# Kernel tuning notes

Measured on AMD Instinct MI355X. Metric: run time of the kernel, lower is better.

Reference implementation:

```python
import jax, jax.numpy as jnp
import numpy as np

N = 50000      # nodes
E = 1600000    # edges (avg degree 32)
C = 48         # num_classes
S = 10         # num_steps


def setup_inputs() -> dict:
    key = jax.random.key(0)
    k1, k2, k3, k4 = jax.random.split(key, 4)
    edge_index = jax.random.randint(k1, (2, E), 0, N)
    edge_attr = jax.random.uniform(k2, (E,), dtype=jnp.float32)  # positive edge weights
    target = jax.random.randint(k3, (N,), 0, C)
    bound = 1.0 / np.sqrt(S)  # uniform(size, weight) init from PyG
    weight = jax.random.uniform(k4, (C, S), minval=-bound, maxval=bound, dtype=jnp.float32)
    return {"edge_index": edge_index, "edge_attr": edge_attr, "target": target, "weight": weight}


def reference(edge_index, edge_attr, target, weight):
    """Adaptive-diffusion random walk: propagate one-hot class indicators
    through a row-normalized weighted transition matrix for S steps and
    combine step-wise landing distributions with learned weight[c, s]."""
    row, col = edge_index[0], edge_index[1]
    # Row-normalize edge weights -> random-walk transition probabilities
    deg = jax.ops.segment_sum(edge_attr, row, num_segments=N)          # [N]
    norm = edge_attr / jnp.clip(deg, 1e-12)[row]                        # [E]
    h0 = jax.nn.one_hot(target, C, dtype=weight.dtype)                  # [N, C]

    def step(h, w_s):
        # message = P^T-style aggregation: scatter src features to dst
        h_new = jax.ops.segment_sum(norm[:, None] * h[row], col, num_segments=N)  # [N, C]
        return h_new, h_new * w_s  # w_s: [C], per-class step coefficient

    _, contribs = jax.lax.scan(step, h0, weight.T)  # contribs: [S, N, C]
    return contribs.sum(0)                          # [N, C]
```

## Files before the change

kernel.cpp:

```cpp
#include <hip/hip_runtime.h>
#include <hip/hip_fp16.h>

#define NN 50000
#define NE 1600000
#define NC 48
#define NS 10
#define PAD 88
#define PADN 50176

#define NBUCK 392
#define NB2   784
#define CAP   4608
#define EPB   2048
#define EPT   2

typedef __attribute__((ext_vector_type(8))) _Float16 half8;

__global__ __launch_bounds__(1024) void bin_kernel(const int* __restrict__ row,
        const int* __restrict__ col, const float* __restrict__ attr,
        int* __restrict__ bcur, uint2* __restrict__ bin, unsigned int* __restrict__ rbin) {
    __shared__ int hcnt[NB2];
    __shared__ int hbase[NB2];
    __shared__ int lofs[NB2];
    __shared__ int sc[1024];
    __shared__ uint2 stageC[EPB];
    __shared__ unsigned int stageR[EPB];
    int tid = threadIdx.x;
    if (tid < NB2) hcnt[tid] = 0;
    __syncthreads();
    int base = blockIdx.x * EPB;
    int ntot = min(EPB, NE - base);
    unsigned int rec[EPT];
    int cv[EPT];
    #pragma unroll
    for (int k = 0; k < EPT; ++k) {
        int e = base + k * 1024 + tid;
        if (e < NE) {
            int r = row[e], c = col[e];
            unsigned int iq = (unsigned int)rintf(attr[e] * 65535.0f);
            rec[k] = (iq << 16) | (unsigned int)r;
            cv[k] = c;
            atomicAdd(&hcnt[c >> 7], 1);
            atomicAdd(&hcnt[NBUCK + (r >> 7)], 1);
        } else {
            cv[k] = -1;
        }
    }
    __syncthreads();
    if (tid < NB2) hbase[tid] = atomicAdd(&bcur[tid], hcnt[tid]);
    sc[tid] = (tid < NB2) ? hcnt[tid] : 0;
    __syncthreads();
    for (int off = 1; off < 1024; off <<= 1) {
        int t = (tid >= off) ? sc[tid - off] : 0;
        __syncthreads();
        sc[tid] += t;
        __syncthreads();
    }
    if (tid < NB2) {
        lofs[tid] = sc[tid] - hcnt[tid];
        hcnt[tid] = 0;
    }
    __syncthreads();
    #pragma unroll
    for (int k = 0; k < EPT; ++k) {
        if (cv[k] >= 0) {
            int b = cv[k] >> 7;
            int rk = atomicAdd(&hcnt[b], 1);
            stageC[lofs[b] + rk] = make_uint2(rec[k], (unsigned int)cv[k]);
            int b2 = NBUCK + ((rec[k] & 0xffffu) >> 7);
            int rk2 = atomicAdd(&hcnt[b2], 1);
            stageR[lofs[b2] + rk2 - ntot] = rec[k];
        }
    }
    __syncthreads();
    for (int i = tid; i < ntot; i += 1024) {
        uint2 rc = stageC[i];
        int b = (int)(rc.y >> 7);
        bin[(size_t)b * CAP + hbase[b] + (i - lofs[b])] = rc;
    }
    for (int i = tid; i < ntot; i += 1024) {
        unsigned int rr = stageR[i];
        int b2 = NBUCK + ((rr & 0xffffu) >> 7);
        rbin[(size_t)(b2 - NBUCK) * CAP + hbase[b2] + (i + ntot - lofs[b2])] = rr;
    }
}

__global__ __launch_bounds__(1024) void degrdeg_kernel(const int* __restrict__ bcur,
        const unsigned int* __restrict__ rbin, const int* __restrict__ target,
        float* __restrict__ rdeg, int2* __restrict__ tq) {
    __shared__ unsigned int acc[128];
    int rb = blockIdx.x;
    if (threadIdx.x < 128) acc[threadIdx.x] = 0;
    __syncthreads();
    int n = bcur[NBUCK + rb];
    const unsigned int* rp = rbin + (size_t)rb * CAP;
    for (int i = threadIdx.x; i < n; i += 1024) {
        unsigned int rr = rp[i];
        atomicAdd(&acc[rr & 127], rr >> 16);
    }
    __syncthreads();
    if (threadIdx.x < 128) {
        int v = (rb << 7) + threadIdx.x;
        if (v < NN) {
            float rd = 65535.0f / fmaxf((float)acc[threadIdx.x], 1.0f);
            rdeg[v] = rd;
            tq[v] = make_int2(target[v], __float_as_int(rd));
        }
    }
}

__global__ __launch_bounds__(1024) void place_kernel(const int* __restrict__ bcur,
        const uint2* __restrict__ bin, unsigned int* __restrict__ edges,
        int* __restrict__ cnt) {
    __shared__ int ccnt[128];
    int b = blockIdx.x;
    if (threadIdx.x < 128) ccnt[threadIdx.x] = 0;
    __syncthreads();
    int n = bcur[b];
    const uint2* rp = bin + (size_t)b * CAP;
    for (int i = threadIdx.x; i < n; i += 1024) {
        uint2 r = rp[i];
        int c = (int)r.y;
        int pos = atomicAdd(&ccnt[c & 127], 1);
        edges[(size_t)c * PAD + pos] = r.x;
    }
    __syncthreads();
    if (threadIdx.x < 128) {
        int c = (b << 7) + threadIdx.x;
        if (c < NN) cnt[c] = ccnt[threadIdx.x];
    }
}

__global__ __launch_bounds__(256) void step1_kernel(const int* __restrict__ cnt,
        const unsigned int* __restrict__ edges, const int2* __restrict__ tq,
        const float* __restrict__ rdeg, const float* __restrict__ weight,
        _Float16* __restrict__ p_new, float* __restrict__ out) {
    int idx = blockIdx.x * blockDim.x + threadIdx.x;
    if (idx >= NN * 6) return;
    int v = idx / 6;
    int q = idx - v * 6;
    int n = cnt[v];
    const unsigned int* ep = edges + (size_t)v * PAD;
    int c0 = 8 * q;
    float a[8] = {0.f, 0.f, 0.f, 0.f, 0.f, 0.f, 0.f, 0.f};
    int i = 0;
    for (; i + 4 <= n; i += 4) {
        uint4 pa = *reinterpret_cast<const uint4*>(ep + i);
        int2 t0 = tq[pa.x & 0xffffu];
        int2 t1 = tq[pa.y & 0xffffu];
        int2 t2 = tq[pa.z & 0xffffu];
        int2 t3 = tq[pa.w & 0xffffu];
        float w0 = (float)(pa.x >> 16) * __int_as_float(t0.y);
        float w1 = (float)(pa.y >> 16) * __int_as_float(t1.y);
        float w2 = (float)(pa.z >> 16) * __int_as_float(t2.y);
        float w3 = (float)(pa.w >> 16) * __int_as_float(t3.y);
        int b0 = t0.x - c0, b1 = t1.x - c0, b2 = t2.x - c0, b3 = t3.x - c0;
        #pragma unroll
        for (int j = 0; j < 8; ++j) {
            a[j] += (b0 == j) ? w0 : 0.f;
            a[j] += (b1 == j) ? w1 : 0.f;
            a[j] += (b2 == j) ? w2 : 0.f;
            a[j] += (b3 == j) ? w3 : 0.f;
        }
    }
    for (; i < n; ++i) {
        unsigned int w_ = ep[i];
        int2 t0 = tq[w_ & 0xffffu];
        float w0 = (float)(w_ >> 16) * __int_as_float(t0.y);
        int b0 = t0.x - c0;
        #pragma unroll
        for (int j = 0; j < 8; ++j) a[j] += (b0 == j) ? w0 : 0.f;
    }
    #pragma unroll
    for (int j = 0; j < 8; ++j) a[j] *= (1.0f / 65535.0f);

    size_t off = (size_t)v * NC + c0;
    float w[8];
    #pragma unroll
    for (int j = 0; j < 8; ++j) w[j] = weight[(c0 + j) * NS + 0];
    *reinterpret_cast<float4*>(out + off) =
        make_float4(a[0] * w[0], a[1] * w[1], a[2] * w[2], a[3] * w[3]);
    *reinterpret_cast<float4*>(out + off + 4) =
        make_float4(a[4] * w[4], a[5] * w[5], a[6] * w[6], a[7] * w[7]);
    float rd = rdeg[v];
    half8 ph;
    #pragma unroll
    for (int j = 0; j < 8; ++j) ph[j] = (_Float16)(a[j] * rd);
    *reinterpret_cast<half8*>(p_new + off) = ph;
}

__device__ __forceinline__ void acc_edge(unsigned int w_, const char* pb, float* a) {
    const half8 g = *reinterpret_cast<const half8*>(pb + (w_ & 0xffffu) * (NC * 2));
    float wv = (float)(w_ >> 16) * (1.0f / 65535.0f);
    #pragma unroll
    for (int j = 0; j < 8; ++j) a[j] += wv * (float)g[j];
}

template <bool LAST>
__global__ __launch_bounds__(256) void gather_kernel(const int* __restrict__ cnt,
        const unsigned int* __restrict__ edges, const float* __restrict__ rdeg,
        const _Float16* __restrict__ p, _Float16* __restrict__ p_new,
        const float* __restrict__ weight, int t, float* __restrict__ out) {
    int idx = blockIdx.x * blockDim.x + threadIdx.x;
    if (idx >= NN * 6) return;
    int v = idx / 6;
    int q = idx - v * 6;
    int n = cnt[v];
    const unsigned int* ep = edges + (size_t)v * PAD;
    const char* pb = (const char*)p + q * 16;
    float a[8] = {0.f, 0.f, 0.f, 0.f, 0.f, 0.f, 0.f, 0.f};
    int i = 0;
    for (; i + 8 <= n; i += 8) {
        uint4 pa = *reinterpret_cast<const uint4*>(ep + i);
        uint4 pc = *reinterpret_cast<const uint4*>(ep + i + 4);
        acc_edge(pa.x, pb, a); acc_edge(pa.y, pb, a);
        acc_edge(pa.z, pb, a); acc_edge(pa.w, pb, a);
        acc_edge(pc.x, pb, a); acc_edge(pc.y, pb, a);
        acc_edge(pc.z, pb, a); acc_edge(pc.w, pb, a);
    }
    for (; i < n; ++i) acc_edge(ep[i], pb, a);

    size_t off = (size_t)v * NC + q * 8;
    int c0 = 8 * q;
    float w[8];
    #pragma unroll
    for (int j = 0; j < 8; ++j) w[j] = weight[(c0 + j) * NS + (t - 1)];
    float* op = out + off;
    float4 o0 = *reinterpret_cast<float4*>(op);
    float4 o1 = *reinterpret_cast<float4*>(op + 4);
    o0.x += a[0] * w[0]; o0.y += a[1] * w[1]; o0.z += a[2] * w[2]; o0.w += a[3] * w[3];
    o1.x += a[4] * w[4]; o1.y += a[5] * w[5]; o1.z += a[6] * w[6]; o1.w += a[7] * w[7];
    *reinterpret_cast<float4*>(op) = o0;
    *reinterpret_cast<float4*>(op + 4) = o1;
    if (!LAST) {
        float rd = rdeg[v];
        half8 ph;
        #pragma unroll
        for (int j = 0; j < 8; ++j) ph[j] = (_Float16)(a[j] * rd);
        *reinterpret_cast<half8*>(p_new + off) = ph;
    }
}

extern "C" void kernel_launch(void* const* d_in, const int* in_sizes, int n_in,
                              void* d_out, int out_size, void* d_ws, size_t ws_size,
                              hipStream_t stream) {
    const int*   edge_index = (const int*)d_in[0];
    const float* edge_attr  = (const float*)d_in[1];
    const int*   target     = (const int*)d_in[2];
    const float* weight     = (const float*)d_in[3];
    float* out = (float*)d_out;

    const int* row = edge_index;
    const int* col = edge_index + NE;

    float*        rdeg  = (float*)d_ws;
    int*          bcur  = (int*)(rdeg + PADN);
    int*          cnt   = bcur + 1024;
    int2*         tq    = (int2*)(cnt + PADN);
    unsigned int* edges = (unsigned int*)(tq + NN);
    unsigned int* rbin  = edges;
    uint2*        bin   = (uint2*)(edges + (size_t)NN * PAD);
    _Float16*     pA    = (_Float16*)((char*)bin + (size_t)NBUCK * CAP * sizeof(uint2)
                                      - (size_t)2 * NN * NC * sizeof(_Float16));
    _Float16*     pB    = pA + (size_t)NN * NC;

    hipMemsetAsync(bcur, 0, 1024 * sizeof(int), stream);

    bin_kernel<<<(NE + EPB - 1) / EPB, 1024, 0, stream>>>(row, col, edge_attr,
            bcur, bin, rbin);
    degrdeg_kernel<<<NBUCK, 1024, 0, stream>>>(bcur, rbin, target, rdeg, tq);
    place_kernel<<<NBUCK, 1024, 0, stream>>>(bcur, bin, edges, cnt);

    const int gblocks = (NN * 6 + 255) / 256;
    _Float16* p = pA;
    _Float16* p_new = pB;
    step1_kernel<<<gblocks, 256, 0, stream>>>(cnt, edges, tq, rdeg, weight, p, out);
    for (int t = 2; t <= NS - 1; ++t) {
        gather_kernel<false><<<gblocks, 256, 0, stream>>>(cnt, edges, rdeg, p, p_new,
                                                          weight, t, out);
        _Float16* tmp = p; p = p_new; p_new = tmp;
    }
    gather_kernel<true><<<gblocks, 256, 0, stream>>>(cnt, edges, rdeg, p, p_new,
                                                     weight, NS, out);
}
```

Before: 395.9 us.

## Sort nodes by in-degree into a permutation to balance gather wavefronts

Adds histogram, scan and permutation kernels that order nodes by their in-degree count, and the step and gather kernels now process nodes through this permutation so lanes in a wavefront have similar loop trip counts. Edge-list loads also become nontemporal. The aim is less divergence and tail imbalance within wavefronts. The cost is three extra small launches, an indirection load per thread, and scattered rather than contiguous access to the output and p arrays. Degrees at or above NDEG (96) would overflow the histogram; this relies on PAD (88) capping the per-node count.

```diff
diff --git a/kernel.cpp b/kernel.cpp
--- a/kernel.cpp
+++ b/kernel.cpp
@@ -13,8 +13,10 @@
 #define CAP   4608
 #define EPB   2048
 #define EPT   2
+#define NDEG  96
 
 typedef __attribute__((ext_vector_type(8))) _Float16 half8;
+typedef __attribute__((ext_vector_type(4))) unsigned int uint4v;
 
 __global__ __launch_bounds__(1024) void bin_kernel(const int* __restrict__ row,
         const int* __restrict__ col, const float* __restrict__ attr,
@@ -131,21 +133,70 @@
     }
 }
 
+__global__ __launch_bounds__(256) void dhist_kernel(const int* __restrict__ cnt,
+        int* __restrict__ dhist) {
+    __shared__ int h[NDEG];
+    if (threadIdx.x < NDEG) h[threadIdx.x] = 0;
+    __syncthreads();
+    int v = blockIdx.x * 256 + threadIdx.x;
+    if (v < NN) atomicAdd(&h[cnt[v]], 1);
+    __syncthreads();
+    if (threadIdx.x < NDEG && h[threadIdx.x]) atomicAdd(&dhist[threadIdx.x], h[threadIdx.x]);
+}
+
+__global__ void dscan_kernel(int* __restrict__ dhist) {
+    __shared__ int s[NDEG];
+    int t = threadIdx.x;
+    int val = (t < NDEG) ? dhist[t] : 0;
+    if (t < NDEG) s[t] = val;
+    __syncthreads();
+    for (int o = 1; o < NDEG; o <<= 1) {
+        int x = (t < NDEG && t >= o) ? s[t - o] : 0;
+        __syncthreads();
+        if (t < NDEG) s[t] += x;
+        __syncthreads();
+    }
+    if (t < NDEG) dhist[t] = s[t] - val;
+}
+
+__global__ __launch_bounds__(256) void perm_kernel(const int* __restrict__ cnt,
+        int* __restrict__ dbase, int* __restrict__ perm) {
+    __shared__ int h[NDEG];
+    __shared__ int base[NDEG];
+    if (threadIdx.x < NDEG) h[threadIdx.x] = 0;
+    __syncthreads();
+    int v = blockIdx.x * 256 + threadIdx.x;
+    int d = (v < NN) ? cnt[v] : -1;
+    if (d >= 0) atomicAdd(&h[d], 1);
+    __syncthreads();
+    if (threadIdx.x < NDEG) {
+        base[threadIdx.x] = h[threadIdx.x] ? atomicAdd(&dbase[threadIdx.x], h[threadIdx.x]) : 0;
+        h[threadIdx.x] = 0;
+    }
+    __syncthreads();
+    if (d >= 0) {
+        int rk = atomicAdd(&h[d], 1);
+        perm[base[d] + rk] = v;
+    }
+}
+
 __global__ __launch_bounds__(256) void step1_kernel(const int* __restrict__ cnt,
+        const int* __restrict__ perm,
         const unsigned int* __restrict__ edges, const int2* __restrict__ tq,
         const float* __restrict__ rdeg, const float* __restrict__ weight,
         _Float16* __restrict__ p_new, float* __restrict__ out) {
     int idx = blockIdx.x * blockDim.x + threadIdx.x;
     if (idx >= NN * 6) return;
-    int v = idx / 6;
-    int q = idx - v * 6;
+    int vslot = idx / 6;
+    int q = idx - vslot * 6;
+    int v = perm[vslot];
     int n = cnt[v];
     const unsigned int* ep = edges + (size_t)v * PAD;
     int c0 = 8 * q;
     float a[8] = {0.f, 0.f, 0.f, 0.f, 0.f, 0.f, 0.f, 0.f};
     int i = 0;
     for (; i + 4 <= n; i += 4) {
-        uint4 pa = *reinterpret_cast<const uint4*>(ep + i);
+        uint4v pa = __builtin_nontemporal_load(reinterpret_cast<const uint4v*>(ep + i));
         int2 t0 = tq[pa.x & 0xffffu];
         int2 t1 = tq[pa.y & 0xffffu];
         int2 t2 = tq[pa.z & 0xffffu];
@@ -198,21 +249,23 @@
 
 template <bool LAST>
 __global__ __launch_bounds__(256) void gather_kernel(const int* __restrict__ cnt,
+        const int* __restrict__ perm,
         const unsigned int* __restrict__ edges, const float* __restrict__ rdeg,
         const _Float16* __restrict__ p, _Float16* __restrict__ p_new,
         const float* __restrict__ weight, int t, float* __restrict__ out) {
     int idx = blockIdx.x * blockDim.x + threadIdx.x;
     if (idx >= NN * 6) return;
-    int v = idx / 6;
-    int q = idx - v * 6;
+    int vslot = idx / 6;
+    int q = idx - vslot * 6;
+    int v = perm[vslot];
     int n = cnt[v];
     const unsigned int* ep = edges + (size_t)v * PAD;
     const char* pb = (const char*)p + q * 16;
     float a[8] = {0.f, 0.f, 0.f, 0.f, 0.f, 0.f, 0.f, 0.f};
     int i = 0;
     for (; i + 8 <= n; i += 8) {
-        uint4 pa = *reinterpret_cast<const uint4*>(ep + i);
-        uint4 pc = *reinterpret_cast<const uint4*>(ep + i + 4);
+        uint4v pa = __builtin_nontemporal_load(reinterpret_cast<const uint4v*>(ep + i));
+        uint4v pc = __builtin_nontemporal_load(reinterpret_cast<const uint4v*>(ep + i + 4));
         acc_edge(pa.x, pb, a); acc_edge(pa.y, pb, a);
         acc_edge(pa.z, pb, a); acc_edge(pa.w, pb, a);
         acc_edge(pc.x, pb, a); acc_edge(pc.y, pb, a);
@@ -255,8 +308,10 @@
 
     float*        rdeg  = (float*)d_ws;
     int*          bcur  = (int*)(rdeg + PADN);
-    int*          cnt   = bcur + 1024;
-    int2*         tq    = (int2*)(cnt + PADN);
+    int*          dhist = bcur + 1024;
+    int*          cnt   = dhist + 128;
+    int*          perm  = cnt + PADN;
+    int2*         tq    = (int2*)(perm + PADN);
     unsigned int* edges = (unsigned int*)(tq + NN);
     unsigned int* rbin  = edges;
     uint2*        bin   = (uint2*)(edges + (size_t)NN * PAD);
@@ -264,22 +319,27 @@
                                       - (size_t)2 * NN * NC * sizeof(_Float16));
     _Float16*     pB    = pA + (size_t)NN * NC;
 
-    hipMemsetAsync(bcur, 0, 1024 * sizeof(int), stream);
+    hipMemsetAsync(bcur, 0, (1024 + 128) * sizeof(int), stream);
 
     bin_kernel<<<(NE + EPB - 1) / EPB, 1024, 0, stream>>>(row, col, edge_attr,
             bcur, bin, rbin);
     degrdeg_kernel<<<NBUCK, 1024, 0, stream>>>(bcur, rbin, target, rdeg, tq);
     place_kernel<<<NBUCK, 1024, 0, stream>>>(bcur, bin, edges, cnt);
 
+    const int nblk = (NN + 255) / 256;
+    dhist_kernel<<<nblk, 256, 0, stream>>>(cnt, dhist);
+    dscan_kernel<<<1, 128, 0, stream>>>(dhist);
+    perm_kernel<<<nblk, 256, 0, stream>>>(cnt, dhist, perm);
+
     const int gblocks = (NN * 6 + 255) / 256;
     _Float16* p = pA;
     _Float16* p_new = pB;
-    step1_kernel<<<gblocks, 256, 0, stream>>>(cnt, edges, tq, rdeg, weight, p, out);
+    step1_kernel<<<gblocks, 256, 0, stream>>>(cnt, perm, edges, tq, rdeg, weight, p, out);
     for (int t = 2; t <= NS - 1; ++t) {
-        gather_kernel<false><<<gblocks, 256, 0, stream>>>(cnt, edges, rdeg, p, p_new,
+        gather_kernel<false><<<gblocks, 256, 0, stream>>>(cnt, perm, edges, rdeg, p, p_new,
                                                           weight, t, out);
         _Float16* tmp = p; p = p_new; p_new = tmp;
     }
-    gather_kernel<true><<<gblocks, 256, 0, stream>>>(cnt, edges, rdeg, p, p_new,
+    gather_kernel<true><<<gblocks, 256, 0, stream>>>(cnt, perm, edges, rdeg, p, p_new,
                                                      weight, NS, out);
 }
```

Result: slower. 478.7 us (+20.9%).

## Split each node's edge list across two threads and combine with shuffle

Applied to the files above, without the earlier changes.

Each (node, 8-class chunk) is now handled by two adjacent threads that each process half of the edge list, with partial sums combined through a lane shuffle. One thread of the pair writes the output accumulation and the other writes the next-step fp16 state, so the stores are split between them. The aim is twice as many threads in flight, more memory-level parallelism on the gathers and a shorter serial edge loop per thread. In exchange the kernels do more index arithmetic and shuffles, and the gather unroll drops from 8 to 4.

```diff
diff --git a/kernel.cpp b/kernel.cpp
--- a/kernel.cpp
+++ b/kernel.cpp
@@ -131,20 +131,30 @@
     }
 }
 
+__device__ __forceinline__ void hrange(int n, int h, int& lo, int& hi) {
+    int mid = 4 * (((n + 3) / 4 + 1) / 2);
+    lo = h ? mid : 0;
+    hi = h ? n : min(mid, n);
+}
+
 __global__ __launch_bounds__(256) void step1_kernel(const int* __restrict__ cnt,
         const unsigned int* __restrict__ edges, const int2* __restrict__ tq,
         const float* __restrict__ rdeg, const float* __restrict__ weight,
         _Float16* __restrict__ p_new, float* __restrict__ out) {
     int idx = blockIdx.x * blockDim.x + threadIdx.x;
-    if (idx >= NN * 6) return;
-    int v = idx / 6;
-    int q = idx - v * 6;
+    if (idx >= NN * 12) return;
+    int v = idx / 12;
+    int r12 = idx - v * 12;
+    int q = r12 >> 1;
+    int h = r12 & 1;
     int n = cnt[v];
     const unsigned int* ep = edges + (size_t)v * PAD;
     int c0 = 8 * q;
     float a[8] = {0.f, 0.f, 0.f, 0.f, 0.f, 0.f, 0.f, 0.f};
-    int i = 0;
-    for (; i + 4 <= n; i += 4) {
+    int lo, hi;
+    hrange(n, h, lo, hi);
+    int i = lo;
+    for (; i + 4 <= hi; i += 4) {
         uint4 pa = *reinterpret_cast<const uint4*>(ep + i);
         int2 t0 = tq[pa.x & 0xffffu];
         int2 t1 = tq[pa.y & 0xffffu];
@@ -163,7 +173,7 @@
             a[j] += (b3 == j) ? w3 : 0.f;
         }
     }
-    for (; i < n; ++i) {
+    for (; i < hi; ++i) {
         unsigned int w_ = ep[i];
         int2 t0 = tq[w_ & 0xffffu];
         float w0 = (float)(w_ >> 16) * __int_as_float(t0.y);
@@ -172,21 +182,26 @@
         for (int j = 0; j < 8; ++j) a[j] += (b0 == j) ? w0 : 0.f;
     }
     #pragma unroll
+    for (int j = 0; j < 8; ++j) a[j] += __shfl_xor(a[j], 1);
+    #pragma unroll
     for (int j = 0; j < 8; ++j) a[j] *= (1.0f / 65535.0f);
 
     size_t off = (size_t)v * NC + c0;
-    float w[8];
-    #pragma unroll
-    for (int j = 0; j < 8; ++j) w[j] = weight[(c0 + j) * NS + 0];
-    *reinterpret_cast<float4*>(out + off) =
-        make_float4(a[0] * w[0], a[1] * w[1], a[2] * w[2], a[3] * w[3]);
-    *reinterpret_cast<float4*>(out + off + 4) =
-        make_float4(a[4] * w[4], a[5] * w[5], a[6] * w[6], a[7] * w[7]);
-    float rd = rdeg[v];
-    half8 ph;
-    #pragma unroll
-    for (int j = 0; j < 8; ++j) ph[j] = (_Float16)(a[j] * rd);
-    *reinterpret_cast<half8*>(p_new + off) = ph;
+    if (h == 0) {
+        float w[8];
+        #pragma unroll
+        for (int j = 0; j < 8; ++j) w[j] = weight[(c0 + j) * NS + 0];
+        *reinterpret_cast<float4*>(out + off) =
+            make_float4(a[0] * w[0], a[1] * w[1], a[2] * w[2], a[3] * w[3]);
+        *reinterpret_cast<float4*>(out + off + 4) =
+            make_float4(a[4] * w[4], a[5] * w[5], a[6] * w[6], a[7] * w[7]);
+    } else {
+        float rd = rdeg[v];
+        half8 ph;
+        #pragma unroll
+        for (int j = 0; j < 8; ++j) ph[j] = (_Float16)(a[j] * rd);
+        *reinterpret_cast<half8*>(p_new + off) = ph;
+    }
 }
 
 __device__ __forceinline__ void acc_edge(unsigned int w_, const char* pb, float* a) {
@@ -202,37 +217,42 @@
         const _Float16* __restrict__ p, _Float16* __restrict__ p_new,
         const float* __restrict__ weight, int t, float* __restrict__ out) {
     int idx = blockIdx.x * blockDim.x + threadIdx.x;
-    if (idx >= NN * 6) return;
-    int v = idx / 6;
-    int q = idx - v * 6;
+    if (idx >= NN * 12) return;
+    int v = idx / 12;
+    int r12 = idx - v * 12;
+    int q = r12 >> 1;
+    int h = r12 & 1;
     int n = cnt[v];
     const unsigned int* ep = edges + (size_t)v * PAD;
     const char* pb = (const char*)p + q * 16;
     float a[8] = {0.f, 0.f, 0.f, 0.f, 0.f, 0.f, 0.f, 0.f};
-    int i = 0;
-    for (; i + 8 <= n; i += 8) {
+    int lo, hi;
+    hrange(n, h, lo, hi);
+    int i = lo;
+    for (; i + 4 <= hi; i += 4) {
         uint4 pa = *reinterpret_cast<const uint4*>(ep + i);
-        uint4 pc = *reinterpret_cast<const uint4*>(ep + i + 4);
         acc_edge(pa.x, pb, a); acc_edge(pa.y, pb, a);
         acc_edge(pa.z, pb, a); acc_edge(pa.w, pb, a);
-        acc_edge(pc.x, pb, a); acc_edge(pc.y, pb, a);
-        acc_edge(pc.z, pb, a); acc_edge(pc.w, pb, a);
-    }
-    for (; i < n; ++i) acc_edge(ep[i], pb, a);
+    }
+    for (; i < hi; ++i) acc_edge(ep[i], pb, a);
+
+    #pragma unroll
+    for (int j = 0; j < 8; ++j) a[j] += __shfl_xor(a[j], 1);
 
     size_t off = (size_t)v * NC + q * 8;
     int c0 = 8 * q;
-    float w[8];
-    #pragma unroll
-    for (int j = 0; j < 8; ++j) w[j] = weight[(c0 + j) * NS + (t - 1)];
-    float* op = out + off;
-    float4 o0 = *reinterpret_cast<float4*>(op);
-    float4 o1 = *reinterpret_cast<float4*>(op + 4);
-    o0.x += a[0] * w[0]; o0.y += a[1] * w[1]; o0.z += a[2] * w[2]; o0.w += a[3] * w[3];
-    o1.x += a[4] * w[4]; o1.y += a[5] * w[5]; o1.z += a[6] * w[6]; o1.w += a[7] * w[7];
-    *reinterpret_cast<float4*>(op) = o0;
-    *reinterpret_cast<float4*>(op + 4) = o1;
-    if (!LAST) {
+    if (h == 0) {
+        float w[8];
+        #pragma unroll
+        for (int j = 0; j < 8; ++j) w[j] = weight[(c0 + j) * NS + (t - 1)];
+        float* op = out + off;
+        float4 o0 = *reinterpret_cast<float4*>(op);
+        float4 o1 = *reinterpret_cast<float4*>(op + 4);
+        o0.x += a[0] * w[0]; o0.y += a[1] * w[1]; o0.z += a[2] * w[2]; o0.w += a[3] * w[3];
+        o1.x += a[4] * w[4]; o1.y += a[5] * w[5]; o1.z += a[6] * w[6]; o1.w += a[7] * w[7];
+        *reinterpret_cast<float4*>(op) = o0;
+        *reinterpret_cast<float4*>(op + 4) = o1;
+    } else if (!LAST) {
         float rd = rdeg[v];
         half8 ph;
         #pragma unroll
@@ -271,7 +291,7 @@
     degrdeg_kernel<<<NBUCK, 1024, 0, stream>>>(bcur, rbin, target, rdeg, tq);
     place_kernel<<<NBUCK, 1024, 0, stream>>>(bcur, bin, edges, cnt);
 
-    const int gblocks = (NN * 6 + 255) / 256;
+    const int gblocks = (NN * 12 + 255) / 256;
     _Float16* p = pA;
     _Float16* p_new = pB;
     step1_kernel<<<gblocks, 256, 0, stream>>>(cnt, edges, tq, rdeg, weight, p, out);
```

Result: slower. 409.2 us (+3.4%).
